# Kernel optimization log

Hardware: AMD Instinct MI355X
Metric: run time of the kernel (lower is better)

## Reference

```python
import jax, jax.numpy as jnp
import numpy as np

B, S, T = 128, 128, 128
E, H = 256, 512
NEG_INF = -1e9


def setup_inputs() -> dict:
    key = jax.random.key(0)
    ks = jax.random.split(key, 12)
    rn = lambda k, sh: (jax.random.normal(k, sh, jnp.float32) * 0.05)
    return {
        "trg_embed": rn(ks[0], (B, T, E)),
        "encoder_hidden": rn(ks[1], (B, S, 2 * H)),
        "encoder_final": rn(ks[2], (1, B, 2 * H)),
        "src_mask": jnp.ones((B, 1, S), bool),
        "trg_mask": jnp.ones((B, T), bool),
        # Bahdanau attention params (Linear, bias=False)
        "W_key": rn(ks[3], (H, 2 * H)),      # key_layer
        "W_query": rn(ks[4], (H, H)),        # query_layer
        "v_energy": rn(ks[5], (H,)),         # energy_layer (H -> 1)
        # GRU cell params (torch layout: gates [r, z, n])
        "W_ih": rn(ks[6], (3 * H, E + 2 * H)),
        "W_hh": rn(ks[7], (3 * H, H)),
        "b_ih": rn(ks[8], (3 * H,)),
        "b_hh": rn(ks[9], (3 * H,)),
        # bridge: Linear(2H -> H, bias=True)
        "W_bridge": rn(ks[10], (H, 2 * H)),
        "b_bridge": jnp.zeros((H,), jnp.float32),
        # pre_output_layer: Linear(H + 2H + E -> H, bias=False)
        "W_preout": rn(ks[11], (H, H + 2 * H + E)),
    }


def reference(trg_embed, encoder_hidden, encoder_final, src_mask, trg_mask,
              W_key, W_query, v_energy, W_ih, W_hh, b_ih, b_hh,
              W_bridge, b_bridge, W_preout):
    # proj_key precomputed once, as in the torch module
    proj_key = jnp.einsum("bsk,hk->bsh", encoder_hidden, W_key)  # [B,S,H]
    # init_hidden: tanh(bridge(encoder_final)); num_layers=1 -> h: [B,H]
    h0 = jnp.tanh(encoder_final[0] @ W_bridge.T + b_bridge)
    mask = src_mask[:, 0, :]  # [B,S]

    def step(h, prev_embed):  # h: [B,H], prev_embed: [B,E]
        # Bahdanau additive attention, query = last-layer hidden
        q = h @ W_query.T  # [B,H]
        scores = jnp.einsum("bsh,h->bs", jnp.tanh(q[:, None, :] + proj_key), v_energy)
        scores = jnp.where(mask, scores, NEG_INF)
        alphas = jax.nn.softmax(scores, axis=-1)
        context = jnp.einsum("bs,bsd->bd", alphas, encoder_hidden)  # [B,2H]
        # single-step GRU (torch gate order r, z, n)
        x = jnp.concatenate([prev_embed, context], axis=-1)  # [B,E+2H]
        gi = x @ W_ih.T + b_ih
        gh = h @ W_hh.T + b_hh
        i_r, i_z, i_n = jnp.split(gi, 3, axis=-1)
        h_r, h_z, h_n = jnp.split(gh, 3, axis=-1)
        r = jax.nn.sigmoid(i_r + h_r)
        z = jax.nn.sigmoid(i_z + h_z)
        n = jnp.tanh(i_n + r * h_n)
        h_new = (1.0 - z) * n + z * h
        # pre-output projection (dropout p=0 / eval mode)
        pre = jnp.concatenate([prev_embed, h_new, context], axis=-1) @ W_preout.T
        return h_new, (h_new, pre)

    xs = jnp.swapaxes(trg_embed, 0, 1)  # [T,B,E]
    hT, (states, preouts) = jax.lax.scan(step, h0, xs)
    decoder_states = jnp.swapaxes(states, 0, 1)      # [B,T,H]
    pre_output_vectors = jnp.swapaxes(preouts, 0, 1)  # [B,T,H]
    hidden = hT[None]  # [1,B,H] to mirror torch layout
    cell_state = jnp.zeros_like(hidden)  # GRU: untouched zeros
    return decoder_states, hidden, pre_output_vectors, cell_state
```

## Files before the change

### kernel.cpp

```cpp
#include <hip/hip_runtime.h>
#include <hip/hip_bf16.h>

typedef __bf16 bf16_t;
typedef __bf16 bf16x8 __attribute__((ext_vector_type(8)));
typedef float  f32x4  __attribute__((ext_vector_type(4)));
typedef float  f32x2  __attribute__((ext_vector_type(2)));
typedef unsigned long long u64;

#define Bx 128
#define Sx 128
#define Tx 128
#define Ex 256
#define Hx 512
#define H2 1024
#define G3 1536
#define KX 1280
#define KP 1792

#define NBLK 256
#define NGRP 16
#define FLAG_OFF 512

#define OUT_STATES 0
#define OUT_HID    8388608
#define OUT_PRE    8454144
#define OUT_CELL   16842752

#define ASCOPE __HIP_MEMORY_SCOPE_AGENT

static __device__ __forceinline__ u64 ald8(const void* p){
  return __hip_atomic_load((const u64*)p, __ATOMIC_RELAXED, ASCOPE);
}
static __device__ __forceinline__ void ast4(void* p, unsigned v){
  __hip_atomic_store((unsigned*)p, v, __ATOMIC_RELAXED, ASCOPE);
}
static __device__ __forceinline__ float aldf(const float* p){
  return __hip_atomic_load(p, __ATOMIC_RELAXED, ASCOPE);
}
static __device__ __forceinline__ void astf(float* p, float v){
  __hip_atomic_store(p, v, __ATOMIC_RELAXED, ASCOPE);
}

__device__ __forceinline__ float fast_tanh(float x){
  float e = __expf(2.0f*x);
  return 1.0f - 2.0f/(e + 1.0f);
}
__device__ __forceinline__ float fast_sigmoid(float x){
  return 1.0f/(1.0f + __expf(-x));
}

__device__ __forceinline__ bf16x8 ld_cvt8(const float* p){
  f32x4 a = *(const f32x4*)p;
  f32x4 b = *(const f32x4*)(p+4);
  bf16x8 r;
  r[0]=(bf16_t)a[0]; r[1]=(bf16_t)a[1]; r[2]=(bf16_t)a[2]; r[3]=(bf16_t)a[3];
  r[4]=(bf16_t)b[0]; r[5]=(bf16_t)b[1]; r[6]=(bf16_t)b[2]; r[7]=(bf16_t)b[3];
  return r;
}

__device__ __forceinline__ void gsync(unsigned* __restrict__ barv, unsigned next,
                                      int tid, int blk){
  __syncthreads();
  if (tid == 0)
    __hip_atomic_fetch_add(&barv[(blk & (NGRP-1))*32], 1u,
                           __ATOMIC_RELAXED, ASCOPE);
  if (blk == 0){
    if (tid < NGRP){
      const unsigned target = next * (NBLK / NGRP);
      while (__hip_atomic_load(&barv[tid*32], __ATOMIC_RELAXED, ASCOPE) < target)
        __builtin_amdgcn_s_sleep(1);
    }
    __syncthreads();
    if (tid < NGRP)
      __hip_atomic_store(&barv[FLAG_OFF + tid*32], next, __ATOMIC_RELAXED, ASCOPE);
  } else if (tid == 0){
    while (__hip_atomic_load(&barv[FLAG_OFF + (blk & (NGRP-1))*32],
                             __ATOMIC_RELAXED, ASCOPE) < next)
      __builtin_amdgcn_s_sleep(2);
  }
  __syncthreads();
}

__global__ void init_bar(unsigned* barv){
  const int i = blockIdx.x*256 + threadIdx.x;
  if (i < FLAG_OFF + NGRP*32)
    __hip_atomic_store(&barv[i], 0u, __ATOMIC_RELAXED, ASCOPE);
}

__global__ void cvt_kernel(const float* __restrict__ in, bf16_t* __restrict__ out, int n){
  const int i = (blockIdx.x*256 + threadIdx.x)*4;
  if (i < n){
    f32x4 v = *(const f32x4*)(in + i);
    bf16_t o[4]; o[0]=(bf16_t)v[0]; o[1]=(bf16_t)v[1]; o[2]=(bf16_t)v[2]; o[3]=(bf16_t)v[3];
    *(ulong1*)(out + i) = *(ulong1*)o;
  }
}

__global__ void bridge_kernel(const float* __restrict__ ef, const float* __restrict__ Wb,
                              const float* __restrict__ bb, float* __restrict__ hf){
  const int b = blockIdx.x;
  const int h = threadIdx.x;
  __shared__ float efs[H2];
  for (int k = threadIdx.x; k < H2; k += blockDim.x) efs[k] = ef[b*H2 + k];
  __syncthreads();
  const float* wrow = Wb + h*H2;
  float acc = bb[h];
  for (int k = 0; k < H2; k += 4){
    f32x4 w = *(const f32x4*)(wrow + k);
    acc += efs[k]*w[0] + efs[k+1]*w[1] + efs[k+2]*w[2] + efs[k+3]*w[3];
  }
  hf[b*Hx + h] = fast_tanh(acc);
}

__global__ void pk_gemm(const float* __restrict__ eh, const bf16_t* __restrict__ Wkb,
                        bf16_t* __restrict__ pk){
  const int gwid = (blockIdx.x*blockDim.x + threadIdx.x) >> 6;
  const int lane = threadIdx.x & 63;
  const int quad = lane >> 4, c = lane & 15;
  const int mt = gwid >> 5;
  const int nt = gwid & 31;
  const float*  pa = eh  + (mt*16 + c)*H2 + quad*8;
  const bf16_t* pb = Wkb + (nt*16 + c)*H2 + quad*8;
  f32x4 acc = {0.f,0.f,0.f,0.f};
  for (int k = 0; k < H2; k += 32)
    acc = __builtin_amdgcn_mfma_f32_16x16x32_bf16(ld_cvt8(pa + k),
                                                  *(const bf16x8*)(pb + k), acc, 0,0,0);
  bf16_t* C = pk + mt*16*Hx + nt*16;
  #pragma unroll
  for (int r = 0; r < 4; r++) C[(quad*4 + r)*Hx + c] = (bf16_t)acc[r];
}

__global__ void __launch_bounds__(512, 2)
loop_kernel(const float* __restrict__ trg, const float* __restrict__ eh,
            const bf16_t* __restrict__ ehb,
            const float* __restrict__ ven, const bf16_t* __restrict__ pk,
            const bf16_t* __restrict__ Wqb, const bf16_t* __restrict__ Whhb,
            const bf16_t* __restrict__ Wihb, const float* __restrict__ bih,
            const float* __restrict__ bhh, const bf16_t* __restrict__ Wpb,
            bf16_t* __restrict__ xbuf, float* __restrict__ qf, float* __restrict__ ghf,
            float* __restrict__ hf,
            float* __restrict__ states, float* __restrict__ pre,
            unsigned* __restrict__ barv){
  const int tid  = threadIdx.x;
  const int lane = tid & 63;
  const int wid  = tid >> 6;
  const int blk  = blockIdx.x;
  const int quad = lane >> 4, c16 = lane & 15;

  const int b    = blk >> 1;
  const int half = blk & 1;

  __shared__ bf16_t shA[16*1280];
  __shared__ f32x4  pacc[3][8][64];
  __shared__ float  red[8][Hx];
  __shared__ float  sc[Sx];
  __shared__ float  smax_s, ssum_s;

  float vv[8];
  *(f32x4*)(vv)   = *(const f32x4*)(ven + lane*8);
  *(f32x4*)(vv+4) = *(const f32x4*)(ven + lane*8 + 4);

  const int mtA   = (blk < 64) ? (blk >> 3) : ((blk*4 - 256)/96);
  const int jobA  = blk*4 + (wid & 3);
  const int khalfA= (wid >> 2)*256;
  unsigned gen = 0;

  for (int t = 0; t < Tx; t++){
    {
      const int row = tid >> 5, c0 = (tid & 31)*16, swr = (row & 7) << 3;
      const float* src = hf + (mtA*16 + row)*Hx + c0;
      bf16_t* dst = shA + row*512;
      #pragma unroll
      for (int i = 0; i < 2; i++){
        union{ u64 u[4]; float f[8]; } U;
        U.u[0]=ald8(src+i*8);   U.u[1]=ald8(src+i*8+2);
        U.u[2]=ald8(src+i*8+4); U.u[3]=ald8(src+i*8+6);
        bf16x8 v;
        #pragma unroll
        for (int j = 0; j < 8; j++) v[j] = (bf16_t)U.f[j];
        *(bf16x8*)(dst + ((c0 + i*8) ^ swr)) = v;
      }
    }
    __syncthreads();
    {
      const int sw = (c16 & 7) << 3;
      const bf16_t* pa = shA + c16*512;
      const bf16_t* pb = (jobA < 256)
        ? Wqb  + ((jobA & 31)*16 + c16)*Hx + quad*8
        : Whhb + (((jobA - 256) % 96)*16 + c16)*Hx + quad*8;
      f32x4 acc = {0.f,0.f,0.f,0.f};
      for (int k = khalfA; k < khalfA + 256; k += 32)
        acc = __builtin_amdgcn_mfma_f32_16x16x32_bf16(
                *(const bf16x8*)(pa + ((quad*8 + k) ^ sw)),
                *(const bf16x8*)(pb + k), acc, 0,0,0);
      pacc[0][wid][lane] = acc;
    }
    __syncthreads();
    if (wid < 4){
      f32x4 acc = pacc[0][wid][lane] + pacc[0][wid+4][lane];
      if (jobA < 256){
        const int nt = jobA & 31;
        #pragma unroll
        for (int r = 0; r < 4; r++)
          astf(qf + (mtA*16 + quad*4 + r)*Hx + nt*16 + c16, acc[r]);
      } else {
        const int nt = (jobA - 256) % 96;
        #pragma unroll
        for (int r = 0; r < 4; r++)
          astf(ghf + (mtA*16 + quad*4 + r)*G3 + nt*16 + c16, acc[r]);
      }
    }
    gsync(barv, ++gen, tid, blk);

    {
      float qv[8];
      #pragma unroll
      for (int i = 0; i < 4; i++){
        union{ u64 u; float f[2]; } Q;
        Q.u = ald8(qf + b*Hx + lane*8 + i*2);
        qv[i*2] = Q.f[0]; qv[i*2+1] = Q.f[1];
      }

      #pragma unroll 4
      for (int j = 0; j < 16; j++){
        const int s = wid*16 + j;
        bf16x8 rw = *(const bf16x8*)(pk + (size_t)(b*Sx + s)*Hx + lane*8);
        float p = 0.f;
        #pragma unroll
        for (int i = 0; i < 8; i++)
          p += fast_tanh(qv[i] + (float)rw[i])*vv[i];
        #pragma unroll
        for (int o = 32; o; o >>= 1) p += __shfl_xor(p, o, 64);
        if (lane == 0) sc[s] = p;
      }
      __syncthreads();
      if (tid < 64){
        float m = fmaxf(sc[tid], sc[tid+64]);
        #pragma unroll
        for (int o = 32; o; o >>= 1) m = fmaxf(m, __shfl_xor(m, o, 64));
        if (tid == 0) smax_s = m;
      }
      __syncthreads();
      if (tid < 128) sc[tid] = __expf(sc[tid] - smax_s);
      __syncthreads();
      if (tid < 64){
        float ssum = sc[tid] + sc[tid+64];
        #pragma unroll
        for (int o = 32; o; o >>= 1) ssum += __shfl_xor(ssum, o, 64);
        if (tid == 0) ssum_s = ssum;
      }
      __syncthreads();

      f32x4 c0v = {0.f,0.f,0.f,0.f}, c1v = {0.f,0.f,0.f,0.f};
      if (ehb){
        const bf16_t* eb = ehb + (size_t)b*Sx*H2 + half*Hx + lane*8;
        #pragma unroll 8
        for (int k = 0; k < 16; k++){
          const int s = (k<<3) + wid;
          const float w = sc[s];
          bf16x8 v = *(const bf16x8*)(eb + (size_t)s*H2);
          c0v[0] += w*(float)v[0]; c0v[1] += w*(float)v[1];
          c0v[2] += w*(float)v[2]; c0v[3] += w*(float)v[3];
          c1v[0] += w*(float)v[4]; c1v[1] += w*(float)v[5];
          c1v[2] += w*(float)v[6]; c1v[3] += w*(float)v[7];
        }
      } else {
        const float* ef2 = eh + (size_t)b*Sx*H2 + half*Hx + lane*8;
        #pragma unroll 4
        for (int k = 0; k < 16; k++){
          const int s = (k<<3) + wid;
          const float w = sc[s];
          f32x4 va = *(const f32x4*)(ef2 + (size_t)s*H2);
          f32x4 vb = *(const f32x4*)(ef2 + (size_t)s*H2 + 4);
          c0v[0] += w*va[0]; c0v[1] += w*va[1]; c0v[2] += w*va[2]; c0v[3] += w*va[3];
          c1v[0] += w*vb[0]; c1v[1] += w*vb[1]; c1v[2] += w*vb[2]; c1v[3] += w*vb[3];
        }
      }
      *(f32x4*)(&red[wid][lane*8])     = c0v;
      *(f32x4*)(&red[wid][lane*8 + 4]) = c1v;
      __syncthreads();
      if (tid < 256){
        const float invs = 1.0f/ssum_s;
        const int d = tid*2;
        float r0 = 0.f, r1 = 0.f;
        #pragma unroll
        for (int w = 0; w < 8; w++){ r0 += red[w][d]; r1 += red[w][d+1]; }
        r0 *= invs; r1 *= invs;
        union{ bf16_t h[2]; unsigned u; } P;
        P.h[0] = (bf16_t)r0; P.h[1] = (bf16_t)r1;
        ast4(xbuf + b*KX + Ex + half*Hx + d, P.u);
      }
      if (half == 0 && tid < 128){
        f32x2 tv = *(const f32x2*)(trg + (size_t)(b*Tx + t)*Ex + tid*2);
        union{ bf16_t h[2]; unsigned u; } E;
        E.h[0] = (bf16_t)tv[0]; E.h[1] = (bf16_t)tv[1];
        ast4(xbuf + b*KX + tid*2, E.u);
      }
    }
    gsync(barv, ++gen, tid, blk);

    if (blk < 64){
      const int mt = blk >> 3;
      {
        const int row = tid >> 5, c0 = (tid & 31)*40, swr = (row & 7) << 3;
        const bf16_t* src = xbuf + (size_t)(mt*16 + row)*KX + c0;
        bf16_t* dst = shA + row*1280;
        #pragma unroll
        for (int i = 0; i < 5; i++){
          union{ u64 u[2]; bf16x8 v; } U;
          U.u[0] = ald8(src + i*8);
          U.u[1] = ald8(src + i*8 + 4);
          *(bf16x8*)(dst + ((c0 + i*8) ^ swr)) = U.v;
        }
      }
      __syncthreads();
      const int ntp = (blk & 7)*4 + (wid & 3);
      const int kb  = (wid >> 2)*640;
      const int sw = (c16 & 7) << 3;
      const bf16_t* pa = shA + c16*1280;
      const bf16_t* B0 = Wihb + (ntp*16 + c16)*KX + quad*8;
      const bf16_t* B1 = B0 + Hx*KX;
      const bf16_t* B2 = B0 + H2*KX;
      f32x4 ar = {0.f,0.f,0.f,0.f}, az = ar, an = ar;
      for (int k = kb; k < kb + 640; k += 32){
        bf16x8 a = *(const bf16x8*)(pa + ((quad*8 + k) ^ sw));
        ar = __builtin_amdgcn_mfma_f32_16x16x32_bf16(a, *(const bf16x8*)(B0+k), ar, 0,0,0);
        az = __builtin_amdgcn_mfma_f32_16x16x32_bf16(a, *(const bf16x8*)(B1+k), az, 0,0,0);
        an = __builtin_amdgcn_mfma_f32_16x16x32_bf16(a, *(const bf16x8*)(B2+k), an, 0,0,0);
      }
      pacc[0][wid][lane] = ar;
      pacc[1][wid][lane] = az;
      pacc[2][wid][lane] = an;
      __syncthreads();
      if (wid < 4){
        f32x4 arT = pacc[0][wid][lane] + pacc[0][wid+4][lane];
        f32x4 azT = pacc[1][wid][lane] + pacc[1][wid+4][lane];
        f32x4 anT = pacc[2][wid][lane] + pacc[2][wid+4][lane];
        const int j = ntp*16 + c16;
        const float bir = bih[j], biz = bih[Hx+j], bin = bih[H2+j];
        const float bhr = bhh[j], bhz = bhh[Hx+j], bhn = bhh[H2+j];
        #pragma unroll
        for (int r = 0; r < 4; r++){
          const int b_ = mt*16 + quad*4 + r;
          const float hr = aldf(ghf + b_*G3 + j)       + bhr;
          const float hz = aldf(ghf + b_*G3 + Hx + j)  + bhz;
          const float hn = aldf(ghf + b_*G3 + H2 + j)  + bhn;
          const float rg = fast_sigmoid(arT[r] + bir + hr);
          const float zg = fast_sigmoid(azT[r] + biz + hz);
          const float ng = fast_tanh(anT[r] + bin + rg*hn);
          const float hold = aldf(hf + b_*Hx + j);
          const float hnew = (1.0f - zg)*ng + zg*hold;
          astf(hf + b_*Hx + j, hnew);
          states[(size_t)(b_*Tx + t)*Hx + j] = hnew;
        }
      }
    } else if (blk < 128){
      const int mt2 = (blk - 64) >> 3;
      {
        const int row = tid >> 5, c0 = (tid & 31)*32, swr = (row & 7) << 3;
        const bf16_t* src = xbuf + (size_t)(mt2*16 + row)*KX + Ex + c0;
        bf16_t* dst = shA + row*1024;
        #pragma unroll
        for (int i = 0; i < 4; i++){
          union{ u64 u[2]; bf16x8 v; } U;
          U.u[0] = ald8(src + i*8);
          U.u[1] = ald8(src + i*8 + 4);
          *(bf16x8*)(dst + ((c0 + i*8) ^ swr)) = U.v;
        }
      }
      __syncthreads();
      const int nt2 = ((blk - 64) & 7)*4 + (wid & 3);
      const int kb  = (wid >> 2)*512;
      const int sw = (c16 & 7) << 3;
      const bf16_t* pa = shA + c16*1024;
      const bf16_t* B = Wpb + (nt2*16 + c16)*KP + (Ex + Hx) + quad*8;
      f32x4 acc = {0.f,0.f,0.f,0.f};
      for (int k = kb; k < kb + 512; k += 32)
        acc = __builtin_amdgcn_mfma_f32_16x16x32_bf16(
                *(const bf16x8*)(pa + ((quad*8 + k) ^ sw)),
                *(const bf16x8*)(B + k), acc, 0,0,0);
      pacc[0][wid][lane] = acc;
      __syncthreads();
      if (wid < 4){
        f32x4 accT = pacc[0][wid][lane] + pacc[0][wid+4][lane];
        #pragma unroll
        for (int r = 0; r < 4; r++){
          const int b_ = mt2*16 + quad*4 + r;
          pre[(size_t)(b_*Tx + t)*Hx + nt2*16 + c16] = accT[r];
        }
      }
    }
    gsync(barv, ++gen, tid, blk);
  }
}

__global__ void preout_gemm(const bf16_t* __restrict__ trgb, const float* __restrict__ states,
                            const bf16_t* __restrict__ Wpb, float* __restrict__ pre){
  const int gwid = (blockIdx.x*blockDim.x + threadIdx.x) >> 6;
  const int lane = threadIdx.x & 63;
  const int quad = lane >> 4, c16 = lane & 15;
  const int mt = gwid >> 5, nt = gwid & 31;
  const int m = mt*16 + c16;
  const bf16_t* Bp = Wpb + (nt*16 + c16)*KP + quad*8;
  f32x4 acc = {0.f,0.f,0.f,0.f};
  const bf16_t* Ae = trgb + m*Ex + quad*8;
  for (int k = 0; k < Ex; k += 32)
    acc = __builtin_amdgcn_mfma_f32_16x16x32_bf16(*(const bf16x8*)(Ae+k),
                                                  *(const bf16x8*)(Bp+k), acc, 0,0,0);
  const float* As = states + m*Hx + quad*8;
  for (int k = 0; k < Hx; k += 32)
    acc = __builtin_amdgcn_mfma_f32_16x16x32_bf16(ld_cvt8(As+k),
                                                  *(const bf16x8*)(Bp+Ex+k), acc, 0,0,0);
  float* C = pre + mt*16*Hx + nt*16;
  #pragma unroll
  for (int r = 0; r < 4; r++){
    const int o = (quad*4 + r)*Hx + c16;
    C[o] = acc[r] + C[o];
  }
}

__global__ void finalize_kernel(const float* __restrict__ hf,
                                float* __restrict__ hid, float* __restrict__ cell){
  const int i = blockIdx.x*256 + threadIdx.x;
  hid[i]  = hf[i];
  cell[i] = 0.0f;
}

extern "C" void kernel_launch(void* const* d_in, const int* in_sizes, int n_in,
                              void* d_out, int out_size, void* d_ws, size_t ws_size,
                              hipStream_t stream){
  int shift = 0;
  for (int i = 0; i < n_in; i++){
    if (in_sizes[i] == 1966080){ shift = i - 8; break; }
  }
  #define IN(k) (((k) < 3) ? d_in[(k)] : d_in[(k) + shift])
  const float* trg = (const float*)IN(0);
  const float* eh  = (const float*)IN(1);
  const float* ef  = (const float*)IN(2);
  const float* Wk  = (const float*)IN(5);
  const float* Wq  = (const float*)IN(6);
  const float* ven = (const float*)IN(7);
  const float* Wih = (const float*)IN(8);
  const float* Whh = (const float*)IN(9);
  const float* bih = (const float*)IN(10);
  const float* bhh = (const float*)IN(11);
  const float* Wb  = (const float*)IN(12);
  const float* bb  = (const float*)IN(13);
  const float* Wp  = (const float*)IN(14);
  #undef IN

  char* ws = (char*)d_ws;
  bf16_t* xbuf = (bf16_t*)(ws + 0);
  float*  hf   = (float* )(ws + 327680);
  float*  qf   = (float* )(ws + 720896);
  float*  ghf  = (float* )(ws + 983040);
  bf16_t* Wkb  = (bf16_t*)(ws + 1769472);
  bf16_t* Wqb  = (bf16_t*)(ws + 2818048);
  bf16_t* Whhb = (bf16_t*)(ws + 3342336);
  bf16_t* Wihb = (bf16_t*)(ws + 4915200);
  bf16_t* Wpb  = (bf16_t*)(ws + 8847360);
  bf16_t* trgb = (bf16_t*)(ws + 10682368);
  bf16_t* pk   = (bf16_t*)(ws + 19070976);

  const size_t EHB_OFF = 35848192;
  const size_t EHB_SZ  = (size_t)Bx*Sx*H2*sizeof(bf16_t);
  bf16_t* ehb = (ws_size >= EHB_OFF + EHB_SZ) ? (bf16_t*)(ws + EHB_OFF) : (bf16_t*)0;

  unsigned* barv = (unsigned*)Wkb;

  float* out    = (float*)d_out;
  float* states = out + OUT_STATES;
  float* hid    = out + OUT_HID;
  float* pre    = out + OUT_PRE;
  float* cell   = out + OUT_CELL;

  cvt_kernel<<<dim3(512),  dim3(256), 0, stream>>>(Wk,  Wkb,  524288);
  cvt_kernel<<<dim3(256),  dim3(256), 0, stream>>>(Wq,  Wqb,  262144);
  cvt_kernel<<<dim3(768),  dim3(256), 0, stream>>>(Whh, Whhb, 786432);
  cvt_kernel<<<dim3(1920), dim3(256), 0, stream>>>(Wih, Wihb, 1966080);
  cvt_kernel<<<dim3(896),  dim3(256), 0, stream>>>(Wp,  Wpb,  917504);
  cvt_kernel<<<dim3(4096), dim3(256), 0, stream>>>(trg, trgb, 4194304);
  if (ehb)
    cvt_kernel<<<dim3(16384), dim3(256), 0, stream>>>(eh, ehb, 16777216);

  bridge_kernel<<<dim3(Bx), dim3(Hx), 0, stream>>>(ef, Wb, bb, hf);
  pk_gemm<<<dim3(8192), dim3(256), 0, stream>>>(eh, Wkb, pk);
  init_bar<<<dim3(4), dim3(256), 0, stream>>>(barv);

  loop_kernel<<<dim3(NBLK), dim3(512), 0, stream>>>(trg, eh, ehb, ven, pk,
                                                    Wqb, Whhb, Wihb, bih, bhh, Wpb,
                                                    xbuf, qf, ghf, hf,
                                                    states, pre, barv);

  preout_gemm<<<dim3(8192), dim3(256), 0, stream>>>(trgb, states, Wpb, pre);
  finalize_kernel<<<dim3(256), dim3(256), 0, stream>>>(hf, hid, cell);
}
```

Before: 7.659 ms.

## Keep per-block proj_key and encoder_hidden slices resident in registers across timesteps

Each block now loads its slice of proj_key and encoder_hidden (converted to bf16) into registers once before the time loop. The attention score and context loops then read those registers instead of reloading from global memory every step. The separate bf16 conversion pass over encoder_hidden and the fallback fp32 path are removed. This adds roughly 128 VGPRs per thread, which risks register spilling or occupancy pressure under the 512x2 launch bounds.

```diff
diff --git a/kernel.cpp b/kernel.cpp
--- a/kernel.cpp
+++ b/kernel.cpp
@@ -132,7 +132,6 @@
 
 __global__ void __launch_bounds__(512, 2)
 loop_kernel(const float* __restrict__ trg, const float* __restrict__ eh,
-            const bf16_t* __restrict__ ehb,
             const float* __restrict__ ven, const bf16_t* __restrict__ pk,
             const bf16_t* __restrict__ Wqb, const bf16_t* __restrict__ Whhb,
             const bf16_t* __restrict__ Wihb, const float* __restrict__ bih,
@@ -160,6 +159,21 @@
   *(f32x4*)(vv)   = *(const f32x4*)(ven + lane*8);
   *(f32x4*)(vv+4) = *(const f32x4*)(ven + lane*8 + 4);
 
+  bf16x8 pkr[16];
+  {
+    const bf16_t* pkb = pk + (size_t)(b*Sx + wid*16)*Hx + lane*8;
+    #pragma unroll
+    for (int j = 0; j < 16; j++)
+      pkr[j] = *(const bf16x8*)(pkb + (size_t)j*Hx);
+  }
+  bf16x8 ehr[16];
+  {
+    const float* ehsrc = eh + (size_t)b*Sx*H2 + half*Hx + lane*8;
+    #pragma unroll
+    for (int k = 0; k < 16; k++)
+      ehr[k] = ld_cvt8(ehsrc + (size_t)((k<<3) + wid)*H2);
+  }
+
   const int mtA   = (blk < 64) ? (blk >> 3) : ((blk*4 - 256)/96);
   const int jobA  = blk*4 + (wid & 3);
   const int khalfA= (wid >> 2)*256;
@@ -221,17 +235,15 @@
         qv[i*2] = Q.f[0]; qv[i*2+1] = Q.f[1];
       }
 
-      #pragma unroll 4
+      #pragma unroll
       for (int j = 0; j < 16; j++){
-        const int s = wid*16 + j;
-        bf16x8 rw = *(const bf16x8*)(pk + (size_t)(b*Sx + s)*Hx + lane*8);
         float p = 0.f;
         #pragma unroll
         for (int i = 0; i < 8; i++)
-          p += fast_tanh(qv[i] + (float)rw[i])*vv[i];
+          p += fast_tanh(qv[i] + (float)pkr[j][i])*vv[i];
         #pragma unroll
         for (int o = 32; o; o >>= 1) p += __shfl_xor(p, o, 64);
-        if (lane == 0) sc[s] = p;
+        if (lane == 0) sc[wid*16 + j] = p;
       }
       __syncthreads();
       if (tid < 64){
@@ -252,29 +264,14 @@
       __syncthreads();
 
       f32x4 c0v = {0.f,0.f,0.f,0.f}, c1v = {0.f,0.f,0.f,0.f};
-      if (ehb){
-        const bf16_t* eb = ehb + (size_t)b*Sx*H2 + half*Hx + lane*8;
-        #pragma unroll 8
-        for (int k = 0; k < 16; k++){
-          const int s = (k<<3) + wid;
-          const float w = sc[s];
-          bf16x8 v = *(const bf16x8*)(eb + (size_t)s*H2);
-          c0v[0] += w*(float)v[0]; c0v[1] += w*(float)v[1];
-          c0v[2] += w*(float)v[2]; c0v[3] += w*(float)v[3];
-          c1v[0] += w*(float)v[4]; c1v[1] += w*(float)v[5];
-          c1v[2] += w*(float)v[6]; c1v[3] += w*(float)v[7];
-        }
-      } else {
-        const float* ef2 = eh + (size_t)b*Sx*H2 + half*Hx + lane*8;
-        #pragma unroll 4
-        for (int k = 0; k < 16; k++){
-          const int s = (k<<3) + wid;
-          const float w = sc[s];
-          f32x4 va = *(const f32x4*)(ef2 + (size_t)s*H2);
-          f32x4 vb = *(const f32x4*)(ef2 + (size_t)s*H2 + 4);
-          c0v[0] += w*va[0]; c0v[1] += w*va[1]; c0v[2] += w*va[2]; c0v[3] += w*va[3];
-          c1v[0] += w*vb[0]; c1v[1] += w*vb[1]; c1v[2] += w*vb[2]; c1v[3] += w*vb[3];
-        }
+      #pragma unroll
+      for (int k = 0; k < 16; k++){
+        const float w = sc[(k<<3) + wid];
+        const bf16x8 v = ehr[k];
+        c0v[0] += w*(float)v[0]; c0v[1] += w*(float)v[1];
+        c0v[2] += w*(float)v[2]; c0v[3] += w*(float)v[3];
+        c1v[0] += w*(float)v[4]; c1v[1] += w*(float)v[5];
+        c1v[2] += w*(float)v[6]; c1v[3] += w*(float)v[7];
       }
       *(f32x4*)(&red[wid][lane*8])     = c0v;
       *(f32x4*)(&red[wid][lane*8 + 4]) = c1v;
@@ -462,10 +459,6 @@
   bf16_t* trgb = (bf16_t*)(ws + 10682368);
   bf16_t* pk   = (bf16_t*)(ws + 19070976);
 
-  const size_t EHB_OFF = 35848192;
-  const size_t EHB_SZ  = (size_t)Bx*Sx*H2*sizeof(bf16_t);
-  bf16_t* ehb = (ws_size >= EHB_OFF + EHB_SZ) ? (bf16_t*)(ws + EHB_OFF) : (bf16_t*)0;
-
   unsigned* barv = (unsigned*)Wkb;
 
   float* out    = (float*)d_out;
@@ -480,14 +473,12 @@
   cvt_kernel<<<dim3(1920), dim3(256), 0, stream>>>(Wih, Wihb, 1966080);
   cvt_kernel<<<dim3(896),  dim3(256), 0, stream>>>(Wp,  Wpb,  917504);
   cvt_kernel<<<dim3(4096), dim3(256), 0, stream>>>(trg, trgb, 4194304);
-  if (ehb)
-    cvt_kernel<<<dim3(16384), dim3(256), 0, stream>>>(eh, ehb, 16777216);
 
   bridge_kernel<<<dim3(Bx), dim3(Hx), 0, stream>>>(ef, Wb, bb, hf);
   pk_gemm<<<dim3(8192), dim3(256), 0, stream>>>(eh, Wkb, pk);
   init_bar<<<dim3(4), dim3(256), 0, stream>>>(barv);
 
-  loop_kernel<<<dim3(NBLK), dim3(512), 0, stream>>>(trg, eh, ehb, ven, pk,
+  loop_kernel<<<dim3(NBLK), dim3(512), 0, stream>>>(trg, eh, ven, pk,
                                                     Wqb, Whhb, Wihb, bih, bhh, Wpb,
                                                     xbuf, qf, ghf, hf,
                                                     states, pre, barv);
```

After: 10.21 ms. 1.33x slower.
